# Kernel optimization log

Hardware: AMD Instinct MI355X
Metric: run time of the kernel (lower is better)

The kernel has to match this reference:

```python
import jax, jax.numpy as jnp
import numpy as np

LSTM = 400   # lstm_size
M = 20       # output_mixture_components
K = 10       # attention_mixture_components
A = 73       # alphabet_size


def setup_inputs() -> dict:
    key = jax.random.key(0)
    ks = jax.random.split(key, 24)
    B, T, U = 128, 800, 64

    def p(k, shape, scale=0.05):
        return jax.random.normal(k, shape, dtype=jnp.float32) * scale

    in1 = 3 + A                 # lstm1 input: [window, x]
    in2 = 3 + LSTM + A          # lstm2 input: [x, h1, window]
    in3 = 3 + 2 * LSTM + A      # lstm3 input: [x, h1, h2, window]

    inp = {
        "inputs": jax.random.normal(ks[0], (B, T, 3), dtype=jnp.float32) * 0.1,
        "char_seq": jax.random.randint(ks[1], (B, U), 0, A),
        "char_seq_lengths": jax.random.randint(ks[2], (B,), U // 2, U + 1),
        "bias": jnp.full((B,), 0.5, dtype=jnp.float32),
        # LSTMCell params (torch layout: gates order i,f,g,o)
        "Wih1": p(ks[3], (4 * LSTM, in1)), "Whh1": p(ks[4], (4 * LSTM, LSTM)),
        "bih1": p(ks[5], (4 * LSTM,)),    "bhh1": p(ks[6], (4 * LSTM,)),
        "Wih2": p(ks[7], (4 * LSTM, in2)), "Whh2": p(ks[8], (4 * LSTM, LSTM)),
        "bih2": p(ks[9], (4 * LSTM,)),    "bhh2": p(ks[10], (4 * LSTM,)),
        "Wih3": p(ks[11], (4 * LSTM, in3)), "Whh3": p(ks[12], (4 * LSTM, LSTM)),
        "bih3": p(ks[13], (4 * LSTM,)),    "bhh3": p(ks[14], (4 * LSTM,)),
        # Attention: h1 -> (alpha_hat, beta_hat, kappa_hat), 3K outputs
        "Wa": p(ks[15], (3 * K, LSTM)), "ba": p(ks[16], (3 * K,)),
        # GMM head: [h1,h2,h3] -> 6M+1 params
        "Wg": p(ks[17], (6 * M + 1, 3 * LSTM)), "bg": p(ks[18], (6 * M + 1,)),
    }
    return inp


def _lstm_cell(x, h, c, Wih, Whh, bih, bhh):
    gates = x @ Wih.T + bih + h @ Whh.T + bhh
    i, f, g, o = jnp.split(gates, 4, axis=-1)
    c = jax.nn.sigmoid(f) * c + jax.nn.sigmoid(i) * jnp.tanh(g)
    h = jax.nn.sigmoid(o) * jnp.tanh(c)
    return h, c


def reference(inputs, char_seq, char_seq_lengths, bias,
              Wih1, Whh1, bih1, bhh1,
              Wih2, Whh2, bih2, bhh2,
              Wih3, Whh3, bih3, bhh3,
              Wa, ba, Wg, bg):
    B, T, _ = inputs.shape
    U = char_seq.shape[1]
    oh = jax.nn.one_hot(char_seq, A, dtype=jnp.float32)            # [B,U,A]
    u = jnp.arange(U, dtype=jnp.float32)                            # [U]
    umask = (u[None, :] < char_seq_lengths[:, None].astype(jnp.float32)).astype(jnp.float32)
    bias_c = bias[:, None]

    def step(carry, x_t):
        h1, c1, h2, c2, h3, c3, window, kappa = carry
        h1, c1 = _lstm_cell(jnp.concatenate([window, x_t], 1), h1, c1, Wih1, Whh1, bih1, bhh1)
        # Gaussian-mixture attention window (Graves 2013)
        ap = h1 @ Wa.T + ba                                         # [B,3K]
        alpha_h, beta_h, kappa_h = jnp.split(ap, 3, axis=1)
        alpha = jnp.exp(alpha_h)
        beta = jnp.exp(beta_h)
        kappa = kappa + jnp.exp(kappa_h)                            # [B,K]
        # phi[b,u] = sum_k alpha exp(-beta (kappa-u)^2)
        g = jnp.exp(-beta[:, :, None] * (kappa[:, :, None] - u) ** 2)  # [B,K,U]
        phi = jnp.einsum('bk,bku->bu', alpha, g) * umask
        window = jnp.einsum('bu,bua->ba', phi, oh)                  # [B,A]
        h2, c2 = _lstm_cell(jnp.concatenate([x_t, h1, window], 1), h2, c2, Wih2, Whh2, bih2, bhh2)
        h3, c3 = _lstm_cell(jnp.concatenate([x_t, h1, h2, window], 1), h3, c3, Wih3, Whh3, bih3, bhh3)
        # GMM output layer with sampling bias
        out = jnp.concatenate([h1, h2, h3], 1) @ Wg.T + bg          # [B,6M+1]
        pi_hat = out[:, :M]
        mus = out[:, M:3 * M]
        sig_hat = out[:, 3 * M:5 * M]
        rho_hat = out[:, 5 * M:6 * M]
        e_hat = out[:, 6 * M:]
        pis = jax.nn.softmax(pi_hat * (1.0 + bias_c), axis=-1)
        sigmas = jnp.exp(sig_hat - bias_c)
        rhos = jnp.tanh(rho_hat)
        es = jax.nn.sigmoid(e_hat)
        return (h1, c1, h2, c2, h3, c3, window, kappa), (pis, sigmas, rhos, mus, es)

    z = lambda d: jnp.zeros((B, d), dtype=jnp.float32)
    carry0 = (z(LSTM), z(LSTM), z(LSTM), z(LSTM), z(LSTM), z(LSTM), z(A), z(K))
    _, outs = jax.lax.scan(step, carry0, jnp.swapaxes(inputs, 0, 1))
    pis, sigmas, rhos, mus, es = (jnp.swapaxes(o, 0, 1) for o in outs)  # [B,T,*]
    return pis, sigmas, rhos, mus, es
```

## Files before the change

### kernel.cpp

```cpp
#include <hip/hip_runtime.h>
#include <stdint.h>

typedef short s8v __attribute__((ext_vector_type(8)));
typedef _Float16 h8v __attribute__((ext_vector_type(8)));
typedef float f4v __attribute__((ext_vector_type(4)));
typedef unsigned short u16;
typedef unsigned int u32;
typedef unsigned long long u64;

#define TT 800
#define BB 128
#define UU 64
#define ALP 73
#define DD 400

#define G_BATCH 32
#define N_CLUS 4
#define N_MEM 50
#define NTHREADS 256

#define CX0 0
#define CX1 32
#define CWIN 64
#define CWINLO 160
#define CH1 256
#define CH2 672
#define CH3 1088
#define ACT_STRIDE 3072

#define NC1 17
#define NC2 30
#define NC3 43
#define NCO 39
#define NCA 13
#define F1 5
#define F2 8
#define F3 11
#define FA 4
#define FO 10

#define ACT_BYTES (32*ACT_STRIDE)
#define H1LO_OFF ACT_BYTES
#define H1LO_STRIDE 896
#define RBUF_OFF (H1LO_OFF + 32*H1LO_STRIDE)
#define ABK_OFF (RBUF_OFF + 16384)
#define WINS_OFF (ABK_OFF + 3840)
#define CHAR_OFF (RBUF_OFF + 32768)
#define LENS_OFF (CHAR_OFF + 2048)
#define BIASC_OFF (LENS_OFF + 128)
#define BCI_OFF (BIASC_OFF + 128)
#define BAS_OFF (BCI_OFF + 384)
#define BGS_OFF (BAS_OFF + 128)
#define LDS_TOTAL (BGS_OFF + 128)

#define OFF_SIG ((size_t)BB*TT*20)
#define OFF_RHO ((size_t)BB*TT*60)
#define OFF_MU  ((size_t)BB*TT*80)
#define OFF_ES  ((size_t)BB*TT*120)

#define MFMA16(A,B,C) __builtin_amdgcn_mfma_f32_16x16x32_f16(__builtin_bit_cast(h8v,(A)),__builtin_bit_cast(h8v,(B)),(C),0,0,0)

#define AST(p,v) __hip_atomic_store((p),(v),__ATOMIC_RELAXED,__HIP_MEMORY_SCOPE_AGENT)
#define ALD(p)   __hip_atomic_load((p),__ATOMIC_RELAXED,__HIP_MEMORY_SCOPE_AGENT)

__device__ __forceinline__ u16 f16b(float x) {
  _Float16 h = (_Float16)x;
  return __builtin_bit_cast(u16, h);
}
__device__ __forceinline__ float f2f(u16 h) {
  return (float)__builtin_bit_cast(_Float16, h);
}
__device__ __forceinline__ float sigm(float x) { return 1.f / (1.f + __expf(-x)); }
__device__ __forceinline__ float tanhe(float x) {
  float e = __expf(-2.f * fabsf(x));
  float r = (1.f - e) / (1.f + e);
  return (x < 0.f) ? -r : r;
}
__device__ __forceinline__ int imin(int a, int b) { return a < b ? a : b; }
__device__ __forceinline__ int lstm_row(int mem, int n, int r) {
  return (n*2 + (r>>3))*400 + mem*8 + (r&7);
}
__device__ __forceinline__ int out_orow(int rc) {
  if (rc < 20) return rc;
  if (rc < 60) return 60 + (rc-20);
  if (rc < 80) return 100 + (rc-60);
  if (rc < 120) return 20 + (rc-80);
  if (rc == 120) return 120;
  return -1;
}
__device__ __forceinline__ s8v gath(const float* W, int ld, int grow, int cb, int valid, int k0) {
  union { s8v v; u16 u[8]; } r;
  #pragma unroll
  for (int j = 0; j < 8; ++j) {
    int k = k0 + j;
    float x = 0.f;
    if (grow >= 0 && k < valid) x = W[(size_t)grow * ld + cb + k];
    r.u[j] = f16b(x);
  }
  return r.v;
}
__device__ __forceinline__ s8v gathlo(const float* W, int ld, int grow, int cb, int valid, int k0) {
  union { s8v v; u16 u[8]; } r;
  #pragma unroll
  for (int j = 0; j < 8; ++j) {
    int k = k0 + j;
    float x = 0.f;
    if (grow >= 0 && k < valid) x = W[(size_t)grow * ld + cb + k];
    u16 hi = f16b(x);
    r.u[j] = f16b(x - f2f(hi));
  }
  return r.v;
}

extern "C" __global__ __launch_bounds__(NTHREADS, 1)
void hwrnn(const float* __restrict__ xin, const int* __restrict__ chq,
           const int* __restrict__ lenq, const float* __restrict__ biasq,
           const float* __restrict__ Wih1, const float* __restrict__ Whh1,
           const float* __restrict__ bih1, const float* __restrict__ bhh1,
           const float* __restrict__ Wih2, const float* __restrict__ Whh2,
           const float* __restrict__ bih2, const float* __restrict__ bhh2,
           const float* __restrict__ Wih3, const float* __restrict__ Whh3,
           const float* __restrict__ bih3, const float* __restrict__ bhh3,
           const float* __restrict__ Wa, const float* __restrict__ ba,
           const float* __restrict__ Wg, const float* __restrict__ bg,
           float* __restrict__ dout, u32* __restrict__ barr,
           u32* __restrict__ h1g, u32* __restrict__ h2g, u32* __restrict__ h3g,
           u32* __restrict__ h1glo)
{
  extern __shared__ __align__(16) char sm[];
  const int tid = threadIdx.x;
  const int wv = tid >> 6;
  const int ln = tid & 63;
  const int cl = blockIdx.x & 3;
  const int mem = blockIdx.x >> 2;
  const int B0 = cl * G_BATCH;

  const int arow = ln & 15;
  const int k0 = (ln >> 4) * 8;
  const int ahi = (ln >> 4) * 16;
  const int axor = (ln & 7) << 4;
  const int rb0 = arow * ACT_STRIDE;
  const int rb1 = (16 + arow) * ACT_STRIDE;
  const int hb0 = H1LO_OFF + arow * H1LO_STRIDE;
  const int hb1 = H1LO_OFF + (16 + arow) * H1LO_STRIDE;
  const f4v az = {0.f, 0.f, 0.f, 0.f};

  for (int i = tid; i * 16 < RBUF_OFF; i += NTHREADS) *(f4v*)(sm + i*16) = az;
  for (int i = tid; i < 32*UU; i += NTHREADS) {
    int b = i >> 6, u = i & 63;
    ((unsigned char*)(sm + CHAR_OFF))[i] = (unsigned char)chq[(B0 + b)*UU + u];
  }
  if (tid < 32) {
    ((int*)(sm + LENS_OFF))[tid] = lenq[B0 + tid];
    ((float*)(sm + BIASC_OFF))[tid] = biasq[B0 + tid];
    ((float*)(sm + BAS_OFF))[tid] = (tid < 30) ? ba[tid] : 0.f;
    float v = 0.f;
    if (mem == 0) { int orow = out_orow(tid); if (orow >= 0) v = bg[orow]; }
    else if (mem >= 1 && mem <= 6 && tid < 16) {
      int orow = out_orow((mem+1)*16 + tid); if (orow >= 0) v = bg[orow];
    }
    ((float*)(sm + BGS_OFF))[tid] = v;
  }
  if (tid < 96) {
    int l = tid >> 5, r = tid & 31;
    int grow = lstm_row(mem, r >> 4, r & 15);
    const float* bi = (l == 0) ? bih1 : (l == 1) ? bih2 : bih3;
    const float* bh = (l == 0) ? bhh1 : (l == 1) ? bhh2 : bhh3;
    ((float*)(sm + BCI_OFF))[l*32 + r] = bi[grow] + bh[grow];
  }

  s8v wf1[F1][2], wf2[F2][2], wf3[F3][2], wfa[FA][2], walo[FA][2], wfo[2][FO];
  #pragma unroll
  for (int i = 0; i < F1; ++i) {
    int c = wv + 4*i;
    #pragma unroll
    for (int n = 0; n < 2; ++n) {
      s8v v = {0,0,0,0,0,0,0,0};
      if (c < NC1) {
        int grow = lstm_row(mem, n, arow);
        if (c == 0)      v = gath(Wih1, 76, grow, 73, 3, k0);
        else if (c <= 3) v = gath(Wih1, 76, grow, (c-1)*32, imin(32, 73-(c-1)*32), k0);
        else             v = gath(Whh1, 400, grow, (c-4)*32, imin(32, 400-(c-4)*32), k0);
      }
      wf1[i][n] = v;
    }
  }
  #pragma unroll
  for (int i = 0; i < F2; ++i) {
    int c = wv + 4*i;
    #pragma unroll
    for (int n = 0; n < 2; ++n) {
      s8v v = {0,0,0,0,0,0,0,0};
      if (c < NC2) {
        int grow = lstm_row(mem, n, arow);
        if (c == 0)       v = gath(Wih2, 476, grow, 0, 3, k0);
        else if (c <= 13) v = gath(Wih2, 476, grow, 3+32*(c-1), imin(32, 400-32*(c-1)), k0);
        else if (c <= 16) v = gath(Wih2, 476, grow, 403+32*(c-14), imin(32, 73-32*(c-14)), k0);
        else              v = gath(Whh2, 400, grow, 32*(c-17), imin(32, 400-32*(c-17)), k0);
      }
      wf2[i][n] = v;
    }
  }
  #pragma unroll
  for (int i = 0; i < F3; ++i) {
    int c = wv + 4*i;
    #pragma unroll
    for (int n = 0; n < 2; ++n) {
      s8v v = {0,0,0,0,0,0,0,0};
      if (c < NC3) {
        int grow = lstm_row(mem, n, arow);
        if (c == 0)       v = gath(Wih3, 876, grow, 0, 3, k0);
        else if (c <= 13) v = gath(Wih3, 876, grow, 3+32*(c-1), imin(32, 400-32*(c-1)), k0);
        else if (c <= 26) v = gath(Wih3, 876, grow, 403+32*(c-14), imin(32, 400-32*(c-14)), k0);
        else if (c <= 29) v = gath(Wih3, 876, grow, 803+32*(c-27), imin(32, 73-32*(c-27)), k0);
        else              v = gath(Whh3, 400, grow, 32*(c-30), imin(32, 400-32*(c-30)), k0);
      }
      wf3[i][n] = v;
    }
  }
  #pragma unroll
  for (int i = 0; i < FA; ++i) {
    int c = wv + 4*i;
    #pragma unroll
    for (int n = 0; n < 2; ++n) {
      s8v v = {0,0,0,0,0,0,0,0}, vl = v;
      if (c < NCA) {
        int rr = n*16 + arow;
        int grow = (rr < 30) ? rr : -1;
        v  = gath  (Wa, 400, grow, 32*c, imin(32, 400-32*c), k0);
        vl = gathlo(Wa, 400, grow, 32*c, imin(32, 400-32*c), k0);
      }
      wfa[i][n] = v; walo[i][n] = vl;
    }
  }
  #pragma unroll
  for (int o = 0; o < 2; ++o) {
    #pragma unroll
    for (int i = 0; i < FO; ++i) {
      s8v v = {0,0,0,0,0,0,0,0};
      int c = wv + 4*i;
      bool have = (mem == 0) || (mem >= 1 && mem <= 6 && o == 0);
      if (have && c < NCO) {
        int ct = (mem == 0) ? o : (mem + 1);
        int grow = out_orow(ct*16 + arow);
        if (c <= 12)      v = gath(Wg, 1200, grow, 32*c, imin(32, 400-32*c), k0);
        else if (c <= 25) v = gath(Wg, 1200, grow, 400+32*(c-13), imin(32, 400-32*(c-13)), k0);
        else              v = gath(Wg, 1200, grow, 800+32*(c-26), imin(32, 400-32*(c-26)), k0);
      }
      wfo[o][i] = v;
    }
  }

  auto LDA0 = [&](int cb2) -> s8v { return *(const s8v*)(sm + rb0 + ((cb2 + ahi) ^ axor)); };
  auto LDA1 = [&](int cb2) -> s8v { return *(const s8v*)(sm + rb1 + ((cb2 + ahi) ^ axor)); };
  auto LDL0 = [&](int cb2) -> s8v { return *(const s8v*)(sm + hb0 + ((cb2 + ahi) ^ axor)); };
  auto LDL1 = [&](int cb2) -> s8v { return *(const s8v*)(sm + hb1 + ((cb2 + ahi) ^ axor)); };
  auto WPART = [&](int slot, f4v a) {
    *(f4v*)(sm + RBUF_OFF + (((slot*4 + wv)*256) + (ln & 15)*16 + (ln >> 4)*4)*4) = a;
  };
  auto RBF = [&](int slot, int w, int col, int row) -> float {
    return ((float*)(sm + RBUF_OFF))[(slot*4 + w)*256 + col*16 + row];
  };
  const int ub = tid >> 3, uu = tid & 7;
  auto LUPD = [&](int sb, int l, float& c, u32* hg, u32* hlo) {
    int mt = ub >> 4, rw = ub & 15;
    const float* bci = (const float*)(sm + BCI_OFF);
    float vi = bci[l*32 + uu], vf = bci[l*32 + 8 + uu];
    float vg = bci[l*32 + 16 + uu], vo = bci[l*32 + 24 + uu];
    #pragma unroll
    for (int w = 0; w < 4; ++w) {
      vi += RBF(sb + mt, w, uu, rw);
      vf += RBF(sb + mt, w, 8 + uu, rw);
      vg += RBF(sb + 2 + mt, w, uu, rw);
      vo += RBF(sb + 2 + mt, w, 8 + uu, rw);
    }
    c = sigm(vf)*c + sigm(vi)*tanhe(vg);
    float h = sigm(vo)*tanhe(c);
    u16 hb = f16b(h);
    float hl = h - f2f(hb);
    float ho = __shfl_xor(h, 1, 64);
    float hlo_o = __shfl_xor(hl, 1, 64);
    if (!(uu & 1)) {
      size_t gi = ((size_t)(B0 + ub)*DD + mem*8 + uu) >> 1;
      u32 pk = (u32)f16b(h) | ((u32)f16b(ho) << 16);
      AST(hg + gi, pk);
      if (hlo) {
        u32 pl = (u32)f16b(hl) | ((u32)f16b(hlo_o) << 16);
        AST(hlo + gi, pl);
      }
    }
  };
  auto STAGEH = [&](const u32* hg, int cbase) {
    for (int idx = tid; idx < 1600; idx += NTHREADS) {
      int b = idx / 50, c16 = idx % 50;
      const u64* p = (const u64*)(hg + (((size_t)(B0 + b)*DD + c16*8) >> 1));
      u64 v0 = ALD(p);
      u64 v1 = ALD(p + 1);
      int off = b*ACT_STRIDE + ((2*(cbase + c16*8)) ^ ((b & 7) << 4));
      *(u64*)(sm + off) = v0;
      *(u64*)(sm + off + 8) = v1;
    }
  };
  auto STAGEHLO = [&](const u32* hg) {
    for (int idx = tid; idx < 1600; idx += NTHREADS) {
      int b = idx / 50, c16 = idx % 50;
      const u64* p = (const u64*)(hg + (((size_t)(B0 + b)*DD + c16*8) >> 1));
      u64 v0 = ALD(p);
      u64 v1 = ALD(p + 1);
      int off = H1LO_OFF + b*H1LO_STRIDE + ((16*c16) ^ ((b & 7) << 4));
      *(u64*)(sm + off) = v0;
      *(u64*)(sm + off + 8) = v1;
    }
  };
  u32* cA = barr + cl*64;
  u32* cB = barr + cl*64 + 32;
  auto ARRIVE = [&](u32* ctr) {
    asm volatile("s_waitcnt vmcnt(0)" ::: "memory");
    __syncthreads();
    if (tid == 0) __hip_atomic_fetch_add(ctr, 1u, __ATOMIC_RELAXED, __HIP_MEMORY_SCOPE_AGENT);
  };
  auto WAITC = [&](u32* ctr, u32 tgt) {
    if (tid == 0) {
      while (ALD(ctr) < tgt) __builtin_amdgcn_s_sleep(2);
    }
    __syncthreads();
  };

  __syncthreads();
  if (tid < 96) {
    int b = tid/3, cc = tid%3;
    float x = xin[((size_t)(B0+b)*TT)*3 + cc];
    int off = b*ACT_STRIDE + ((2*(CX0 + cc)) ^ ((b&7)<<4));
    *(u16*)(sm + off) = f16b(x);
  }
  __syncthreads();

  float c1 = 0.f, c2 = 0.f, c3 = 0.f, kap0 = 0.f, kap1 = 0.f;

  for (int t = 0; t <= TT; ++t) {
    const int pc = t & 1, pp = pc ^ 1;
    const int xc = pc ? CX1 : CX0;
    const int xp = pp ? CX1 : CX0;

    if (t < TT) {
      f4v a1[4] = {az, az, az, az};
      #pragma unroll
      for (int i = 0; i < F1; ++i) {
        int c = wv + 4*i;
        if (c < NC1) {
          int cb = (c == 0) ? xc : (c <= 3) ? (CWIN + 32*(c-1)) : (CH1 + 32*(c-4));
          int cb2 = 2*cb;
          s8v x0 = LDA0(cb2), x1 = LDA1(cb2);
          a1[0] = MFMA16(x0, wf1[i][0], a1[0]);
          a1[1] = MFMA16(x1, wf1[i][0], a1[1]);
          a1[2] = MFMA16(x0, wf1[i][1], a1[2]);
          a1[3] = MFMA16(x1, wf1[i][1], a1[3]);
          if (c >= 1) {
            s8v l0, l1;
            if (c <= 3) { int lb2 = 2*(CWINLO + 32*(c-1)); l0 = LDA0(lb2); l1 = LDA1(lb2); }
            else        { int lb2 = 64*(c-4);              l0 = LDL0(lb2); l1 = LDL1(lb2); }
            a1[0] = MFMA16(l0, wf1[i][0], a1[0]);
            a1[1] = MFMA16(l1, wf1[i][0], a1[1]);
            a1[2] = MFMA16(l0, wf1[i][1], a1[2]);
            a1[3] = MFMA16(l1, wf1[i][1], a1[3]);
          }
        }
      }
      WPART(0, a1[0]); WPART(1, a1[1]); WPART(2, a1[2]); WPART(3, a1[3]);
    }

    if (t >= 1) WAITC(cB, (u32)t * N_MEM); else __syncthreads();
    if (t >= 1) STAGEH(h2g, CH2);
    __syncthreads();

    if (t < TT) LUPD(0, 0, c1, h1g, h1glo);
    if (t >= 1) {
      f4v a3[4] = {az, az, az, az};
      #pragma unroll
      for (int i = 0; i < F3; ++i) {
        int c = wv + 4*i;
        if (c < NC3) {
          int cb = (c == 0) ? xp
                 : (c <= 13) ? (CH1 + 32*(c-1))
                 : (c <= 26) ? (CH2 + 32*(c-14))
                 : (c <= 29) ? (CWIN + 32*(c-27))
                 : (CH3 + 32*(c-30));
          int cb2 = 2*cb;
          s8v x0 = LDA0(cb2), x1 = LDA1(cb2);
          a3[0] = MFMA16(x0, wf3[i][0], a3[0]);
          a3[1] = MFMA16(x1, wf3[i][0], a3[1]);
          a3[2] = MFMA16(x0, wf3[i][1], a3[2]);
          a3[3] = MFMA16(x1, wf3[i][1], a3[3]);
          if ((c >= 1 && c <= 13) || (c >= 27 && c <= 29)) {
            s8v l0, l1;
            if (c <= 13) { int lb2 = 64*(c-1);               l0 = LDL0(lb2); l1 = LDL1(lb2); }
            else         { int lb2 = 2*(CWINLO + 32*(c-27)); l0 = LDA0(lb2); l1 = LDA1(lb2); }
            a3[0] = MFMA16(l0, wf3[i][0], a3[0]);
            a3[1] = MFMA16(l1, wf3[i][0], a3[1]);
            a3[2] = MFMA16(l0, wf3[i][1], a3[2]);
            a3[3] = MFMA16(l1, wf3[i][1], a3[3]);
          }
        }
      }
      WPART(4, a3[0]); WPART(5, a3[1]); WPART(6, a3[2]); WPART(7, a3[3]);
    }
    __syncthreads();
    if (t >= 1) LUPD(4, 2, c3, h3g, nullptr);

    ARRIVE(cA);

    if (t + 1 < TT) {
      if (tid < 96) {
        int b = tid/3, cc = tid%3;
        float x = xin[((size_t)(B0+b)*TT + (t+1))*3 + cc];
        int off = b*ACT_STRIDE + ((2*(xp + cc)) ^ ((b&7)<<4));
        *(u16*)(sm + off) = f16b(x);
      }
    }

    f4v a2[4] = {az, az, az, az};
    if (t < TT) {
      #pragma unroll
      for (int i = 0; i < F2; ++i) {
        int c = wv + 4*i;
        if (c < NC2 && (c == 0 || c >= 17)) {
          int cb = (c == 0) ? xc : (CH2 + 32*(c-17));
          int cb2 = 2*cb;
          s8v x0 = LDA0(cb2), x1 = LDA1(cb2);
          a2[0] = MFMA16(x0, wf2[i][0], a2[0]);
          a2[1] = MFMA16(x1, wf2[i][0], a2[1]);
          a2[2] = MFMA16(x0, wf2[i][1], a2[2]);
          a2[3] = MFMA16(x1, wf2[i][1], a2[3]);
        }
      }
    }

    WAITC(cA, (u32)(t+1) * N_MEM);

    if (t >= 1) STAGEH(h3g, CH3);
    __syncthreads();

    if (t >= 1 && mem <= 6) {
      f4v ao[4] = {az, az, az, az};
      #pragma unroll
      for (int i = 0; i < FO; ++i) {
        int c = wv + 4*i;
        if (c < NCO) {
          int cb = (c <= 12) ? (CH1 + 32*c)
                 : (c <= 25) ? (CH2 + 32*(c-13))
                 : (CH3 + 32*(c-26));
          int cb2 = 2*cb;
          s8v x0 = LDA0(cb2), x1 = LDA1(cb2);
          ao[0] = MFMA16(x0, wfo[0][i], ao[0]);
          ao[1] = MFMA16(x1, wfo[0][i], ao[1]);
          if (mem == 0) {
            ao[2] = MFMA16(x0, wfo[1][i], ao[2]);
            ao[3] = MFMA16(x1, wfo[1][i], ao[3]);
          }
        }
      }
      WPART(4, ao[0]); WPART(5, ao[1]);
      if (mem == 0) { WPART(6, ao[2]); WPART(7, ao[3]); }
    }
    __syncthreads();

    if (t >= 1 && mem <= 6) {
      const float* bgs = (const float*)(sm + BGS_OFF);
      const float* bcv = (const float*)(sm + BIASC_OFF);
      int tt = t - 1;
      auto OSUM = [&](int rl, int b) -> float {
        int slot = 4 + ((mem == 0) ? ((rl >> 4)*2) : 0) + (b >> 4);
        float s = bgs[rl];
        #pragma unroll
        for (int w = 0; w < 4; ++w) s += RBF(slot, w, rl & 15, b & 15);
        return s;
      };
      if (mem == 0) {
        if (tid < 32) {
          int b = tid;
          float sc = 1.f + bcv[b];
          float pv[20]; float mx = -3e38f;
          #pragma unroll
          for (int r = 0; r < 20; ++r) { pv[r] = OSUM(r, b) * sc; mx = fmaxf(mx, pv[r]); }
          float den = 0.f;
          #pragma unroll
          for (int r = 0; r < 20; ++r) { pv[r] = __expf(pv[r] - mx); den += pv[r]; }
          float inv = 1.f / den;
          size_t ob = ((size_t)(B0 + b)*TT + tt);
          #pragma unroll
          for (int r = 0; r < 20; ++r) dout[ob*20 + r] = pv[r] * inv;
        }
        for (int idx = tid; idx < 12*32; idx += NTHREADS) {
          int rl = 20 + (idx >> 5), b = idx & 31;
          float v = OSUM(rl, b);
          size_t ob = ((size_t)(B0 + b)*TT + tt);
          dout[OFF_SIG + ob*40 + (rl - 20)] = __expf(v - bcv[b]);
        }
      } else {
        int RB = (mem + 1) * 16;
        for (int idx = tid; idx < 512; idx += NTHREADS) {
          int rl = idx >> 5, b = idx & 31;
          int rc = RB + rl;
          float v = OSUM(rl, b);
          size_t ob = ((size_t)(B0 + b)*TT + tt);
          if (rc < 60)        dout[OFF_SIG + ob*40 + (rc - 20)] = __expf(v - bcv[b]);
          else if (rc < 80)   dout[OFF_RHO + ob*20 + (rc - 60)] = tanhe(v);
          else if (rc < 120)  dout[OFF_MU  + ob*40 + (rc - 80)] = v;
          else if (rc == 120) dout[OFF_ES + ob] = sigm(v);
        }
      }
    }
    if (t < TT) { STAGEH(h1g, CH1); STAGEHLO(h1glo); }
    __syncthreads();

    if (t < TT) {
      f4v aa[4] = {az, az, az, az};
      #pragma unroll
      for (int i = 0; i < FA; ++i) {
        int c = wv + 4*i;
        if (c < NCA) {
          int cb2 = 2*(CH1 + 32*c);
          int lb2 = 64*c;
          s8v x0 = LDA0(cb2), x1 = LDA1(cb2);
          s8v l0 = LDL0(lb2), l1 = LDL1(lb2);
          aa[0] = MFMA16(x0, wfa[i][0], aa[0]);
          aa[1] = MFMA16(x1, wfa[i][0], aa[1]);
          aa[2] = MFMA16(x0, wfa[i][1], aa[2]);
          aa[3] = MFMA16(x1, wfa[i][1], aa[3]);
          aa[0] = MFMA16(l0, wfa[i][0], aa[0]);
          aa[1] = MFMA16(l1, wfa[i][0], aa[1]);
          aa[2] = MFMA16(l0, wfa[i][1], aa[2]);
          aa[3] = MFMA16(l1, wfa[i][1], aa[3]);
          aa[0] = MFMA16(x0, walo[i][0], aa[0]);
          aa[1] = MFMA16(x1, walo[i][0], aa[1]);
          aa[2] = MFMA16(x0, walo[i][1], aa[2]);
          aa[3] = MFMA16(x1, walo[i][1], aa[3]);
        }
      }
      WPART(0, aa[0]); WPART(1, aa[1]); WPART(2, aa[2]); WPART(3, aa[3]);
      float* wins = (float*)(sm + WINS_OFF);
      for (int i = tid; i < 32*80; i += NTHREADS) wins[i] = 0.f;
      __syncthreads();

      float* abk = (float*)(sm + ABK_OFF);
      const float* bas = (const float*)(sm + BAS_OFF);
      #pragma unroll
      for (int half = 0; half < 2; ++half) {
        int idx = tid + half*NTHREADS;
        if (idx < 320) {
          int b = idx & 31, j = idx >> 5;
          float ah = bas[j], bh = bas[10+j], kh = bas[20+j];
          #pragma unroll
          for (int w = 0; w < 4; ++w) {
            ah += RBF(0 + (b>>4), w, j, b & 15);
            if (j < 6) bh += RBF(0 + (b>>4), w, 10 + j, b & 15);
            else       bh += RBF(2 + (b>>4), w, j - 6, b & 15);
            kh += RBF(2 + (b>>4), w, 4 + j, b & 15);
          }
          float& kp = half ? kap1 : kap0;
          kp += __expf(kh);
          abk[0*320 + b*10 + j] = __expf(ah);
          abk[1*320 + b*10 + j] = __expf(bh);
          abk[2*320 + b*10 + j] = kp;
        }
      }
      __syncthreads();

      const unsigned char* chs = (const unsigned char*)(sm + CHAR_OFF);
      const int* lns = (const int*)(sm + LENS_OFF);
      for (int idx = tid; idx < 32*64; idx += NTHREADS) {
        int b = idx >> 6, u = idx & 63;
        if (u < lns[b]) {
          float ph = 0.f, fu = (float)u;
          #pragma unroll
          for (int j = 0; j < 10; ++j) {
            float d = abk[2*320 + b*10 + j] - fu;
            ph += abk[0*320 + b*10 + j] * __expf(-abk[1*320 + b*10 + j]*d*d);
          }
          atomicAdd(&wins[b*80 + (int)chs[b*64 + u]], ph);
        }
      }
      __syncthreads();

      for (int idx = tid; idx < 32*96; idx += NTHREADS) {
        int b = idx / 96, cc = idx % 96;
        float v = (cc < ALP) ? wins[b*80 + cc] : 0.f;
        u16 hi = f16b(v);
        u16 lo = f16b(v - f2f(hi));
        int sw = (b&7) << 4;
        *(u16*)(sm + b*ACT_STRIDE + ((2*(CWIN + cc)) ^ sw)) = hi;
        *(u16*)(sm + b*ACT_STRIDE + ((2*(CWINLO + cc)) ^ sw)) = lo;
      }
      __syncthreads();

      #pragma unroll
      for (int i = 0; i < F2; ++i) {
        int c = wv + 4*i;
        if (c >= 1 && c <= 16) {
          int cb = (c <= 13) ? (CH1 + 32*(c-1)) : (CWIN + 32*(c-14));
          int cb2 = 2*cb;
          s8v x0 = LDA0(cb2), x1 = LDA1(cb2);
          a2[0] = MFMA16(x0, wf2[i][0], a2[0]);
          a2[1] = MFMA16(x1, wf2[i][0], a2[1]);
          a2[2] = MFMA16(x0, wf2[i][1], a2[2]);
          a2[3] = MFMA16(x1, wf2[i][1], a2[3]);
          s8v l0, l1;
          if (c <= 13) { int lb2 = 64*(c-1);               l0 = LDL0(lb2); l1 = LDL1(lb2); }
          else         { int lb2 = 2*(CWINLO + 32*(c-14)); l0 = LDA0(lb2); l1 = LDA1(lb2); }
          a2[0] = MFMA16(l0, wf2[i][0], a2[0]);
          a2[1] = MFMA16(l1, wf2[i][0], a2[1]);
          a2[2] = MFMA16(l0, wf2[i][1], a2[2]);
          a2[3] = MFMA16(l1, wf2[i][1], a2[3]);
        }
      }
      WPART(0, a2[0]); WPART(1, a2[1]); WPART(2, a2[2]); WPART(3, a2[3]);
      __syncthreads();
      LUPD(0, 1, c2, h2g, nullptr);
      ARRIVE(cB);
    }
  }
}

extern "C" void kernel_launch(void* const* d_in, const int* in_sizes, int n_in,
                              void* d_out, int out_size, void* d_ws, size_t ws_size,
                              hipStream_t stream) {
  (void)in_sizes; (void)n_in; (void)out_size; (void)ws_size;
  const float* xin  = (const float*)d_in[0];
  const int*   chq  = (const int*)d_in[1];
  const int*   lnq  = (const int*)d_in[2];
  const float* bq   = (const float*)d_in[3];
  const float* Wih1 = (const float*)d_in[4];
  const float* Whh1 = (const float*)d_in[5];
  const float* bih1 = (const float*)d_in[6];
  const float* bhh1 = (const float*)d_in[7];
  const float* Wih2 = (const float*)d_in[8];
  const float* Whh2 = (const float*)d_in[9];
  const float* bih2 = (const float*)d_in[10];
  const float* bhh2 = (const float*)d_in[11];
  const float* Wih3 = (const float*)d_in[12];
  const float* Whh3 = (const float*)d_in[13];
  const float* bih3 = (const float*)d_in[14];
  const float* bhh3 = (const float*)d_in[15];
  const float* Wa   = (const float*)d_in[16];
  const float* ba   = (const float*)d_in[17];
  const float* Wg   = (const float*)d_in[18];
  const float* bg   = (const float*)d_in[19];
  float* dout = (float*)d_out;
  char* ws = (char*)d_ws;
  u32* barr  = (u32*)ws;
  u32* h1g   = (u32*)(ws + 4096);
  u32* h2g   = (u32*)(ws + 4096 + 102400);
  u32* h3g   = (u32*)(ws + 4096 + 204800);
  u32* h1glo = (u32*)(ws + 4096 + 307200);

  hipMemsetAsync(ws, 0, 4096, stream);
  hipFuncSetAttribute(reinterpret_cast<const void*>(hwrnn),
                      hipFuncAttributeMaxDynamicSharedMemorySize, LDS_TOTAL);
  hipLaunchKernelGGL(hwrnn, dim3(N_CLUS * N_MEM), dim3(NTHREADS), LDS_TOTAL, stream,
                     xin, chq, lnq, bq, Wih1, Whh1, bih1, bhh1, Wih2, Whh2, bih2, bhh2,
                     Wih3, Whh3, bih3, bhh3, Wa, ba, Wg, bg, dout, barr, h1g, h2g, h3g,
                     h1glo);
}
```

Before: 19.05 ms.

## Restructure timestep pipeline to use a single grid barrier with ring-buffered hidden states

Removes the second cross-block barrier (cB) per timestep by double-buffering h2/h3/h1lo in global memory and holding h1 in a 4-deep ring. The GMM output layer is delayed by one more step (t-2) and reads h1 straight from the ring in global memory, while layer 3's update is moved later in the step. This cuts each timestep from two grid-wide waits to one, at the cost of an extra pipeline step, larger workspace, and global loads in the output GEMM. The spin-wait sleep interval is also shortened.

```diff
diff --git a/kernel.cpp b/kernel.cpp
--- a/kernel.cpp
+++ b/kernel.cpp
@@ -58,6 +58,8 @@
 #define OFF_MU  ((size_t)BB*TT*80)
 #define OFF_ES  ((size_t)BB*TT*120)
 
+#define HBUF_U32 25600
+
 #define MFMA16(A,B,C) __builtin_amdgcn_mfma_f32_16x16x32_f16(__builtin_bit_cast(h8v,(A)),__builtin_bit_cast(h8v,(B)),(C),0,0,0)
 
 #define AST(p,v) __hip_atomic_store((p),(v),__ATOMIC_RELAXED,__HIP_MEMORY_SCOPE_AGENT)
@@ -124,7 +126,7 @@
            const float* __restrict__ Wa, const float* __restrict__ ba,
            const float* __restrict__ Wg, const float* __restrict__ bg,
            float* __restrict__ dout, u32* __restrict__ barr,
-           u32* __restrict__ h1g, u32* __restrict__ h2g, u32* __restrict__ h3g,
+           u32* __restrict__ h1ring, u32* __restrict__ h2g, u32* __restrict__ h3g,
            u32* __restrict__ h1glo)
 {
   extern __shared__ __align__(16) char sm[];
@@ -261,6 +263,12 @@
   auto RBF = [&](int slot, int w, int col, int row) -> float {
     return ((float*)(sm + RBUF_OFF))[(slot*4 + w)*256 + col*16 + row];
   };
+  auto RLD = [&](const u32* ring, int half) -> s8v {
+    union { s8v v; u64 q[2]; } r;
+    r.q[0] = ALD((const u64*)ring + ((size_t)(B0 + arow + 16*half)*DD + k0 >> 2));
+    r.q[1] = ALD((const u64*)ring + ((size_t)(B0 + arow + 16*half)*DD + k0 + 4 >> 2));
+    return r.v;
+  };
   const int ub = tid >> 3, uu = tid & 7;
   auto LUPD = [&](int sb, int l, float& c, u32* hg, u32* hlo) {
     int mt = ub >> 4, rw = ub & 15;
@@ -313,7 +321,6 @@
     }
   };
   u32* cA = barr + cl*64;
-  u32* cB = barr + cl*64 + 32;
   auto ARRIVE = [&](u32* ctr) {
     asm volatile("s_waitcnt vmcnt(0)" ::: "memory");
     __syncthreads();
@@ -321,7 +328,7 @@
   };
   auto WAITC = [&](u32* ctr, u32 tgt) {
     if (tid == 0) {
-      while (ALD(ctr) < tgt) __builtin_amdgcn_s_sleep(2);
+      while (ALD(ctr) < tgt) __builtin_amdgcn_s_sleep(1);
     }
     __syncthreads();
   };
@@ -337,10 +344,12 @@
 
   float c1 = 0.f, c2 = 0.f, c3 = 0.f, kap0 = 0.f, kap1 = 0.f;
 
-  for (int t = 0; t <= TT; ++t) {
+  for (int t = 0; t <= TT + 1; ++t) {
     const int pc = t & 1, pp = pc ^ 1;
     const int xc = pc ? CX1 : CX0;
     const int xp = pp ? CX1 : CX0;
+    u32* ring_w = h1ring + (size_t)(t & 3) * HBUF_U32;
+    const u32* ring_o = h1ring + (size_t)((t + 2) & 3) * HBUF_U32;
 
     if (t < TT) {
       f4v a1[4] = {az, az, az, az};
@@ -368,13 +377,93 @@
       }
       WPART(0, a1[0]); WPART(1, a1[1]); WPART(2, a1[2]); WPART(3, a1[3]);
     }
-
-    if (t >= 1) WAITC(cB, (u32)t * N_MEM); else __syncthreads();
-    if (t >= 1) STAGEH(h2g, CH2);
-    __syncthreads();
-
-    if (t < TT) LUPD(0, 0, c1, h1g, h1glo);
-    if (t >= 1) {
+    __syncthreads();
+    if (t < TT) LUPD(0, 0, c1, ring_w, h1glo + (size_t)pc * HBUF_U32);
+    ARRIVE(cA);
+
+    WAITC(cA, (u32)(t + 1) * N_MEM);
+
+    if (t >= 2) STAGEH(h3g + (size_t)pc * HBUF_U32, CH3);
+    __syncthreads();
+
+    if (t >= 2 && mem <= 6) {
+      f4v ao[4] = {az, az, az, az};
+      #pragma unroll
+      for (int i = 0; i < FO; ++i) {
+        int c = wv + 4*i;
+        if (c < NCO) {
+          s8v x0, x1;
+          if (c <= 12) {
+            const u32* rp = ring_o + (size_t)c * 16;
+            x0 = RLD(rp, 0); x1 = RLD(rp, 1);
+          } else {
+            int cb = (c <= 25) ? (CH2 + 32*(c-13)) : (CH3 + 32*(c-26));
+            x0 = LDA0(2*cb); x1 = LDA1(2*cb);
+          }
+          ao[0] = MFMA16(x0, wfo[0][i], ao[0]);
+          ao[1] = MFMA16(x1, wfo[0][i], ao[1]);
+          if (mem == 0) {
+            ao[2] = MFMA16(x0, wfo[1][i], ao[2]);
+            ao[3] = MFMA16(x1, wfo[1][i], ao[3]);
+          }
+        }
+      }
+      WPART(4, ao[0]); WPART(5, ao[1]);
+      if (mem == 0) { WPART(6, ao[2]); WPART(7, ao[3]); }
+    }
+    __syncthreads();
+
+    if (t >= 1 && t <= TT) STAGEH(h2g + (size_t)pp * HBUF_U32, CH2);
+    if (t >= 2 && mem <= 6) {
+      const float* bgs = (const float*)(sm + BGS_OFF);
+      const float* bcv = (const float*)(sm + BIASC_OFF);
+      int tt = t - 2;
+      auto OSUM = [&](int rl, int b) -> float {
+        int slot = 4 + ((mem == 0) ? ((rl >> 4)*2) : 0) + (b >> 4);
+        float s = bgs[rl];
+        #pragma unroll
+        for (int w = 0; w < 4; ++w) s += RBF(slot, w, rl & 15, b & 15);
+        return s;
+      };
+      if (mem == 0) {
+        if (tid < 32) {
+          int b = tid;
+          float sc = 1.f + bcv[b];
+          float pv[20]; float mx = -3e38f;
+          #pragma unroll
+          for (int r = 0; r < 20; ++r) { pv[r] = OSUM(r, b) * sc; mx = fmaxf(mx, pv[r]); }
+          float den = 0.f;
+          #pragma unroll
+          for (int r = 0; r < 20; ++r) { pv[r] = __expf(pv[r] - mx); den += pv[r]; }
+          float inv = 1.f / den;
+          size_t ob = ((size_t)(B0 + b)*TT + tt);
+          #pragma unroll
+          for (int r = 0; r < 20; ++r) dout[ob*20 + r] = pv[r] * inv;
+        }
+        for (int idx = tid; idx < 12*32; idx += NTHREADS) {
+          int rl = 20 + (idx >> 5), b = idx & 31;
+          float v = OSUM(rl, b);
+          size_t ob = ((size_t)(B0 + b)*TT + tt);
+          dout[OFF_SIG + ob*40 + (rl - 20)] = __expf(v - bcv[b]);
+        }
+      } else {
+        int RB = (mem + 1) * 16;
+        for (int idx = tid; idx < 512; idx += NTHREADS) {
+          int rl = idx >> 5, b = idx & 31;
+          int rc = RB + rl;
+          float v = OSUM(rl, b);
+          size_t ob = ((size_t)(B0 + b)*TT + tt);
+          if (rc < 60)        dout[OFF_SIG + ob*40 + (rc - 20)] = __expf(v - bcv[b]);
+          else if (rc < 80)   dout[OFF_RHO + ob*20 + (rc - 60)] = tanhe(v);
+          else if (rc < 120)  dout[OFF_MU  + ob*40 + (rc - 80)] = v;
+          else if (rc == 120) dout[OFF_ES + ob] = sigm(v);
+        }
+      }
+    }
+    __syncthreads();
+
+    f4v a2[4] = {az, az, az, az};
+    if (t >= 1 && t <= TT) {
       f4v a3[4] = {az, az, az, az};
       #pragma unroll
       for (int i = 0; i < F3; ++i) {
@@ -404,21 +493,6 @@
       }
       WPART(4, a3[0]); WPART(5, a3[1]); WPART(6, a3[2]); WPART(7, a3[3]);
     }
-    __syncthreads();
-    if (t >= 1) LUPD(4, 2, c3, h3g, nullptr);
-
-    ARRIVE(cA);
-
-    if (t + 1 < TT) {
-      if (tid < 96) {
-        int b = tid/3, cc = tid%3;
-        float x = xin[((size_t)(B0+b)*TT + (t+1))*3 + cc];
-        int off = b*ACT_STRIDE + ((2*(xp + cc)) ^ ((b&7)<<4));
-        *(u16*)(sm + off) = f16b(x);
-      }
-    }
-
-    f4v a2[4] = {az, az, az, az};
     if (t < TT) {
       #pragma unroll
       for (int i = 0; i < F2; ++i) {
@@ -434,83 +508,15 @@
         }
       }
     }
-
-    WAITC(cA, (u32)(t+1) * N_MEM);
-
-    if (t >= 1) STAGEH(h3g, CH3);
-    __syncthreads();
-
-    if (t >= 1 && mem <= 6) {
-      f4v ao[4] = {az, az, az, az};
-      #pragma unroll
-      for (int i = 0; i < FO; ++i) {
-        int c = wv + 4*i;
-        if (c < NCO) {
-          int cb = (c <= 12) ? (CH1 + 32*c)
-                 : (c <= 25) ? (CH2 + 32*(c-13))
-                 : (CH3 + 32*(c-26));
-          int cb2 = 2*cb;
-          s8v x0 = LDA0(cb2), x1 = LDA1(cb2);
-          ao[0] = MFMA16(x0, wfo[0][i], ao[0]);
-          ao[1] = MFMA16(x1, wfo[0][i], ao[1]);
-          if (mem == 0) {
-            ao[2] = MFMA16(x0, wfo[1][i], ao[2]);
-            ao[3] = MFMA16(x1, wfo[1][i], ao[3]);
-          }
-        }
-      }
-      WPART(4, ao[0]); WPART(5, ao[1]);
-      if (mem == 0) { WPART(6, ao[2]); WPART(7, ao[3]); }
-    }
-    __syncthreads();
-
-    if (t >= 1 && mem <= 6) {
-      const float* bgs = (const float*)(sm + BGS_OFF);
-      const float* bcv = (const float*)(sm + BIASC_OFF);
-      int tt = t - 1;
-      auto OSUM = [&](int rl, int b) -> float {
-        int slot = 4 + ((mem == 0) ? ((rl >> 4)*2) : 0) + (b >> 4);
-        float s = bgs[rl];
-        #pragma unroll
-        for (int w = 0; w < 4; ++w) s += RBF(slot, w, rl & 15, b & 15);
-        return s;
-      };
-      if (mem == 0) {
-        if (tid < 32) {
-          int b = tid;
-          float sc = 1.f + bcv[b];
-          float pv[20]; float mx = -3e38f;
-          #pragma unroll
-          for (int r = 0; r < 20; ++r) { pv[r] = OSUM(r, b) * sc; mx = fmaxf(mx, pv[r]); }
-          float den = 0.f;
-          #pragma unroll
-          for (int r = 0; r < 20; ++r) { pv[r] = __expf(pv[r] - mx); den += pv[r]; }
-          float inv = 1.f / den;
-          size_t ob = ((size_t)(B0 + b)*TT + tt);
-          #pragma unroll
-          for (int r = 0; r < 20; ++r) dout[ob*20 + r] = pv[r] * inv;
-        }
-        for (int idx = tid; idx < 12*32; idx += NTHREADS) {
-          int rl = 20 + (idx >> 5), b = idx & 31;
-          float v = OSUM(rl, b);
-          size_t ob = ((size_t)(B0 + b)*TT + tt);
-          dout[OFF_SIG + ob*40 + (rl - 20)] = __expf(v - bcv[b]);
-        }
-      } else {
-        int RB = (mem + 1) * 16;
-        for (int idx = tid; idx < 512; idx += NTHREADS) {
-          int rl = idx >> 5, b = idx & 31;
-          int rc = RB + rl;
-          float v = OSUM(rl, b);
-          size_t ob = ((size_t)(B0 + b)*TT + tt);
-          if (rc < 60)        dout[OFF_SIG + ob*40 + (rc - 20)] = __expf(v - bcv[b]);
-          else if (rc < 80)   dout[OFF_RHO + ob*20 + (rc - 60)] = tanhe(v);
-          else if (rc < 120)  dout[OFF_MU  + ob*40 + (rc - 80)] = v;
-          else if (rc == 120) dout[OFF_ES + ob] = sigm(v);
-        }
-      }
-    }
-    if (t < TT) { STAGEH(h1g, CH1); STAGEHLO(h1glo); }
+    __syncthreads();
+
+    if (t < TT) { STAGEH(ring_w, CH1); STAGEHLO(h1glo + (size_t)pc * HBUF_U32); }
+    if (t + 1 < TT && tid < 96) {
+      int b = tid/3, cc = tid%3;
+      float x = xin[((size_t)(B0+b)*TT + (t+1))*3 + cc];
+      int off = b*ACT_STRIDE + ((2*(xp + cc)) ^ ((b&7)<<4));
+      *(u16*)(sm + off) = f16b(x);
+    }
     __syncthreads();
 
     if (t < TT) {
@@ -538,10 +544,13 @@
         }
       }
       WPART(0, aa[0]); WPART(1, aa[1]); WPART(2, aa[2]); WPART(3, aa[3]);
+    }
+    if (t >= 1 && t <= TT) LUPD(4, 2, c3, h3g + (size_t)pp * HBUF_U32, nullptr);
+    __syncthreads();
+
+    if (t < TT) {
       float* wins = (float*)(sm + WINS_OFF);
       for (int i = tid; i < 32*80; i += NTHREADS) wins[i] = 0.f;
-      __syncthreads();
-
       float* abk = (float*)(sm + ABK_OFF);
       const float* bas = (const float*)(sm + BAS_OFF);
       #pragma unroll
@@ -615,8 +624,8 @@
       }
       WPART(0, a2[0]); WPART(1, a2[1]); WPART(2, a2[2]); WPART(3, a2[3]);
       __syncthreads();
-      LUPD(0, 1, c2, h2g, nullptr);
-      ARRIVE(cB);
+
+      LUPD(0, 1, c2, h2g + (size_t)pc * HBUF_U32, nullptr);
     }
   }
 }
@@ -647,17 +656,17 @@
   const float* bg   = (const float*)d_in[19];
   float* dout = (float*)d_out;
   char* ws = (char*)d_ws;
-  u32* barr  = (u32*)ws;
-  u32* h1g   = (u32*)(ws + 4096);
-  u32* h2g   = (u32*)(ws + 4096 + 102400);
-  u32* h3g   = (u32*)(ws + 4096 + 204800);
-  u32* h1glo = (u32*)(ws + 4096 + 307200);
+  u32* barr   = (u32*)ws;
+  u32* h1ring = (u32*)(ws + 4096);
+  u32* h2g    = (u32*)(ws + 4096 + 409600);
+  u32* h3g    = (u32*)(ws + 4096 + 409600 + 204800);
+  u32* h1glo  = (u32*)(ws + 4096 + 409600 + 409600);
 
   hipMemsetAsync(ws, 0, 4096, stream);
   hipFuncSetAttribute(reinterpret_cast<const void*>(hwrnn),
                       hipFuncAttributeMaxDynamicSharedMemorySize, LDS_TOTAL);
   hipLaunchKernelGGL(hwrnn, dim3(N_CLUS * N_MEM), dim3(NTHREADS), LDS_TOTAL, stream,
                      xin, chq, lnq, bq, Wih1, Whh1, bih1, bhh1, Wih2, Whh2, bih2, bhh2,
-                     Wih3, Whh3, bih3, bhh3, Wa, ba, Wg, bg, dout, barr, h1g, h2g, h3g,
-                     h1glo);
-}
+                     Wih3, Whh3, bih3, bhh3, Wa, ba, Wg, bg, dout, barr,
+                     h1ring, h2g, h3g, h1glo);
+}
```

New measurement: 20.14 ms. 5.7% more time.
